# Performance work log

Measured on AMD Instinct MI355X. Metric: run time of the kernel, lower is better.

Reference implementation:

```python
import jax, jax.numpy as jnp
import numpy as np


def _run_lstm(x, W, U, b, mask=None):
    """Keras-style LSTM returning final hidden state.
    x: [N, T, D] float; W: [D, 4u]; U: [u, 4u]; b: [4u]; mask: [N, T] bool or None.
    Gate order i, f, g(c), o as in Keras. Masked steps carry state through.
    """
    N, T, D = x.shape
    units = U.shape[0]
    xt = jnp.transpose(x, (1, 0, 2))  # [T, N, D]
    if mask is not None:
        mt = jnp.transpose(mask, (1, 0))[:, :, None]  # [T, N, 1]
        xs = (xt, mt)
    else:
        xs = xt

    def step(carry, inp):
        h, c = carry
        if mask is not None:
            x_t, m = inp
        else:
            x_t = inp
        z = x_t @ W + h @ U + b  # [N, 4u]
        i, f, g, o = jnp.split(z, 4, axis=-1)
        i = jax.nn.sigmoid(i)
        f = jax.nn.sigmoid(f)
        g = jnp.tanh(g)
        o = jax.nn.sigmoid(o)
        c_new = f * c + i * g
        h_new = o * jnp.tanh(c_new)
        if mask is not None:
            h_new = jnp.where(m, h_new, h)
            c_new = jnp.where(m, c_new, c)
        return (h_new, c_new), None

    h0 = jnp.zeros((N, units), dtype=x.dtype)
    c0 = jnp.zeros((N, units), dtype=x.dtype)
    (hT, _), _ = jax.lax.scan(step, (h0, c0), xs)
    return hT


def setup_inputs() -> dict:
    key = jax.random.key(0)
    ks = jax.random.split(key, 10)
    B, T, S, D = 256, 256, 20, 1
    U1, U2 = 32, 24  # inner / outer LSTM units
    sc = 0.1
    x = jax.random.normal(ks[0], (B, T, S, D), dtype=jnp.float32)
    lengths = jax.random.randint(ks[1], (B,), 1, T + 1, dtype=jnp.int32)
    Wi = jax.random.normal(ks[2], (D, 4 * U1), dtype=jnp.float32) * sc
    Ui = jax.random.normal(ks[3], (U1, 4 * U1), dtype=jnp.float32) * sc
    bi = jnp.zeros((4 * U1,), dtype=jnp.float32)
    Wo = jax.random.normal(ks[4], (U1, 4 * U2), dtype=jnp.float32) * sc
    Uo = jax.random.normal(ks[5], (U2, 4 * U2), dtype=jnp.float32) * sc
    bo = jnp.zeros((4 * U2,), dtype=jnp.float32)
    Wd = jax.random.normal(ks[6], (U2, 1), dtype=jnp.float32) * sc
    bd = jnp.zeros((1,), dtype=jnp.float32)
    return {"x": x, "lengths": lengths, "Wi": Wi, "Ui": Ui, "bi": bi,
            "Wo": Wo, "Uo": Uo, "bo": bo, "Wd": Wd, "bd": bd}


def reference(x, lengths, Wi, Ui, bi, Wo, Uo, bo, Wd, bd):
    B, T, S, D = x.shape
    # TimeDistributed(LSTM(32)): run inner LSTM over each outer step (inference, dropout off)
    rows = x.reshape(B * T, S, D)
    h_inner = _run_lstm(rows, Wi, Ui, bi)          # [B*T, 32]
    feats = h_inner.reshape(B, T, -1)              # [B, T, 32]
    # Outer LSTM(24) with ragged-length mask (Keras mask semantics: carry state)
    mask = jnp.arange(T)[None, :] < lengths[:, None]  # [B, T]
    h_outer = _run_lstm(feats, Wo, Uo, bo, mask)   # [B, 24]
    # Dense sigmoid head
    return jax.nn.sigmoid(h_outer @ Wd + bd)       # [B, 1]
```

## Files before the change

kernel.cpp:

```cpp
#include <hip/hip_runtime.h>

#define B_  256
#define T_  256
#define S_  20
#define U1  32
#define G1  128
#define U2  24
#define G2  96
#define NT  16

typedef __attribute__((ext_vector_type(8))) short short8;
typedef __attribute__((ext_vector_type(4))) float f32x4;
typedef __attribute__((ext_vector_type(2))) float f32x2;

#define KSIG  (-1.44269504f)
#define KTANH ( 2.88539008f)

__device__ __forceinline__ float sigmoidf_(float x) {
    return __builtin_amdgcn_rcpf(1.0f + __builtin_amdgcn_exp2f(x * KSIG));
}
__device__ __forceinline__ float tanhf_fast(float x) {
    return 1.0f - 2.0f * __builtin_amdgcn_rcpf(1.0f + __builtin_amdgcn_exp2f(x * KTANH));
}
__device__ __forceinline__ float dpp_xor1(float x) {
    return __int_as_float(__builtin_amdgcn_update_dpp(
        0, __float_as_int(x), 0xB1, 0xF, 0xF, true));
}
__device__ __forceinline__ f32x2 dexp2(f32x2 z, float k) {
    f32x2 t = z * k;
    f32x2 e;
    e.x = __builtin_amdgcn_exp2f(t.x);
    e.y = __builtin_amdgcn_exp2f(t.y);
    return e + 1.0f;
}
__device__ __forceinline__ void brcp4(f32x2 d01, f32x2 d23, f32x2& s01, f32x2& s23) {
    const f32x2 m = d01 * d23;
    f32x2 R;
    R.x = __builtin_amdgcn_rcpf(m.x);
    R.y = __builtin_amdgcn_rcpf(m.y);
    s01 = R * d23;
    s23 = R * d01;
}

__device__ __forceinline__ unsigned short f2bf(float a) {
    unsigned int u = __float_as_uint(a);
    u += 0x7FFFu + ((u >> 16) & 1u);
    return (unsigned short)(u >> 16);
}
__device__ __forceinline__ unsigned int pack2bf(float a, float b) {
    unsigned int ua = __float_as_uint(a); ua += 0x7FFFu + ((ua >> 16) & 1u);
    unsigned int ub = __float_as_uint(b); ub += 0x7FFFu + ((ub >> 16) & 1u);
    return (ua >> 16) | (ub & 0xFFFF0000u);
}
union frag_u { short8 v; unsigned int u[4]; };
union h2x  { unsigned int u32; _Float16 h[2]; };

__global__ __attribute__((amdgpu_flat_work_group_size(512, 512)))
__attribute__((amdgpu_waves_per_eu(2, 2)))
void fused_kernel(
    const float* __restrict__ x,
    const int*   __restrict__ lengths,
    const float* __restrict__ Wi,
    const float* __restrict__ Ui,
    const float* __restrict__ bi,
    const float* __restrict__ Wo,
    const float* __restrict__ Uo,
    const float* __restrict__ bo,
    const float* __restrict__ Wd,
    const float* __restrict__ bd,
    float* __restrict__ out)
{
    __shared__ __align__(16) _Float16      Pl[T_][G2];
    __shared__ __align__(16) unsigned short hbb[8][16][40];
    __shared__ unsigned int flags[NT];
    const int b    = blockIdx.x;
    const int len  = lengths[b];
    const int tid  = threadIdx.x;
    const int w    = __builtin_amdgcn_readfirstlane(tid >> 6);
    const int lane = tid & 63;
    const int q    = lane >> 4;
    const int n    = lane & 15;

    if (tid < NT) flags[tid] = 0;
    __syncthreads();

    if (w <= 3) __builtin_amdgcn_s_setprio(2);

    frag_u Bui[8];
#pragma unroll
    for (int tt = 0; tt < 8; ++tt)
#pragma unroll
        for (int k2 = 0; k2 < 4; ++k2)
            Bui[tt].u[k2] = pack2bf(Ui[(8 * q + 2 * k2) * G1 + 16 * tt + n],
                                    Ui[(8 * q + 2 * k2 + 1) * G1 + 16 * tt + n]);
    frag_u Bwo[6];
#pragma unroll
    for (int tt = 0; tt < 6; ++tt)
#pragma unroll
        for (int k2 = 0; k2 < 4; ++k2)
            Bwo[tt].u[k2] = pack2bf(Wo[(8 * q + 2 * k2) * G2 + 16 * tt + n],
                                    Wo[(8 * q + 2 * k2 + 1) * G2 + 16 * tt + n]);
    float bi_l[8], Wi_l[8], bo_l[6];
#pragma unroll
    for (int tt = 0; tt < 8; ++tt) { bi_l[tt] = bi[16 * tt + n]; Wi_l[tt] = Wi[16 * tt + n]; }
#pragma unroll
    for (int tt = 0; tt < 6; ++tt) bo_l[tt] = bo[16 * tt + n];
    int pcol[6];
#pragma unroll
    for (int tt = 0; tt < 6; ++tt) {
        const int col = 16 * tt + n;
        const int g = col / 24;
        pcol[tt] = (col - 24 * g) * 4 + g;
    }

    int tl[3]; int ntl;
    if (w == 0)      { tl[0] = 0; tl[1] = 0; tl[2] = 0; ntl = 1; }
    else if (w == 1) { tl[0] = 1; tl[1] = 8; tl[2] = 9; ntl = 3; }
    else             { tl[0] = w; tl[1] = w + 8; tl[2] = 0; ntl = 2; }

#pragma unroll 1
    for (int i = 0; i < ntl; ++i) {
        const int tile = tl[i];
        const int wt0  = tile * 16;
        if (wt0 >= len) break;

        const float* xr = x + (size_t)(b * T_ + wt0 + 4 * q) * S_;
        f32x2 c01[2], c23[2];
#pragma unroll
        for (int uh = 0; uh < 2; ++uh) { c01[uh] = {0.0f, 0.0f}; c23[uh] = {0.0f, 0.0f}; }

        auto activate = [&](f32x4* acc) {
#pragma unroll
            for (int uh = 0; uh < 2; ++uh) {
                const f32x2 zi01 = { acc[0 + uh][0], acc[0 + uh][1] };
                const f32x2 zi23 = { acc[0 + uh][2], acc[0 + uh][3] };
                const f32x2 zf01 = { acc[2 + uh][0], acc[2 + uh][1] };
                const f32x2 zf23 = { acc[2 + uh][2], acc[2 + uh][3] };
                const f32x2 zg01 = { acc[4 + uh][0], acc[4 + uh][1] };
                const f32x2 zg23 = { acc[4 + uh][2], acc[4 + uh][3] };
                const f32x2 zo01 = { acc[6 + uh][0], acc[6 + uh][1] };
                const f32x2 zo23 = { acc[6 + uh][2], acc[6 + uh][3] };

                f32x2 si01, si23, sf01, sf23, rg01, rg23, so01, so23;
                brcp4(dexp2(zi01, KSIG),  dexp2(zi23, KSIG),  si01, si23);
                brcp4(dexp2(zf01, KSIG),  dexp2(zf23, KSIG),  sf01, sf23);
                brcp4(dexp2(zg01, KTANH), dexp2(zg23, KTANH), rg01, rg23);
                brcp4(dexp2(zo01, KSIG),  dexp2(zo23, KSIG),  so01, so23);
                const f32x2 g01 = 1.0f - 2.0f * rg01;
                const f32x2 g23 = 1.0f - 2.0f * rg23;
                c01[uh] = sf01 * c01[uh] + si01 * g01;
                c23[uh] = sf23 * c23[uh] + si23 * g23;
                f32x2 rc01, rc23;
                brcp4(dexp2(c01[uh], KTANH), dexp2(c23[uh], KTANH), rc01, rc23);
                const f32x2 t01 = 1.0f - 2.0f * rc01;
                const f32x2 t23 = 1.0f - 2.0f * rc23;
                const f32x2 h01 = so01 * t01;
                const f32x2 h23 = so23 * t23;
                hbb[w][4 * q + 0][n + 16 * uh] = f2bf(h01.x);
                hbb[w][4 * q + 1][n + 16 * uh] = f2bf(h01.y);
                hbb[w][4 * q + 2][n + 16 * uh] = f2bf(h23.x);
                hbb[w][4 * q + 3][n + 16 * uh] = f2bf(h23.y);
            }
        };

        float xc[4];
#pragma unroll
        for (int r = 0; r < 4; ++r) xc[r] = xr[r * S_];

        {
            f32x4 acc[8];
#pragma unroll
            for (int tt = 0; tt < 8; ++tt)
#pragma unroll
                for (int r = 0; r < 4; ++r)
                    acc[tt][r] = bi_l[tt] + xc[r] * Wi_l[tt];
            activate(acc);
        }
#pragma unroll
        for (int r = 0; r < 4; ++r) xc[r] = xr[r * S_ + 1];

#pragma unroll 1
        for (int s = 1; s < S_; ++s) {
            const int sn = (s + 1 < S_) ? s + 1 : S_ - 1;
            float xnx[4];
#pragma unroll
            for (int r = 0; r < 4; ++r) xnx[r] = xr[r * S_ + sn];

            f32x4 acc[8];
#pragma unroll
            for (int tt = 0; tt < 8; ++tt)
#pragma unroll
                for (int r = 0; r < 4; ++r)
                    acc[tt][r] = bi_l[tt] + xc[r] * Wi_l[tt];

            const short8 A = *(const short8*)&hbb[w][n][8 * q];
#pragma unroll
            for (int tt = 0; tt < 8; ++tt)
                acc[tt] = __builtin_amdgcn_mfma_f32_16x16x32_bf16(A, Bui[tt].v, acc[tt], 0, 0, 0);

            activate(acc);
#pragma unroll
            for (int r = 0; r < 4; ++r) xc[r] = xnx[r];
        }

        {
            const short8 A = *(const short8*)&hbb[w][n][8 * q];
            f32x4 accp[6];
#pragma unroll
            for (int tt = 0; tt < 6; ++tt) {
#pragma unroll
                for (int r = 0; r < 4; ++r) accp[tt][r] = bo_l[tt];
                accp[tt] = __builtin_amdgcn_mfma_f32_16x16x32_bf16(A, Bwo[tt].v, accp[tt], 0, 0, 0);
            }
#pragma unroll
            for (int r = 0; r < 4; ++r) {
                const int tr = wt0 + 4 * q + r;
#pragma unroll
                for (int tt = 0; tt < 6; ++tt)
                    Pl[tr][pcol[tt]] = (_Float16)accp[tt][r];
            }
        }
        __hip_atomic_store(&flags[tile], 1u, __ATOMIC_RELEASE, __HIP_MEMORY_SCOPE_WORKGROUP);
        if (i == 0) {
            if (w == 0) __builtin_amdgcn_s_setprio(1);
            else        __builtin_amdgcn_s_setprio(0);
        }
    }

    if (w != 0) return;

    const int p = lane & 1;
    const int u = (lane < 2 * U2) ? (lane >> 1) : (U2 - 1);
    const int cA = p ? (2 * U2 + u) : u;
    const int cB = p ? (3 * U2 + u) : (U2 + u);

    const f32x2 kAB = { p ? KTANH : KSIG, KSIG };
    const f32x2 mAB = { p ? -2.0f : 1.0f, 1.0f };
    const f32x2 aAB = { p ?  1.0f : 0.0f, 0.0f };

    auto gates2 = [&](f32x2 z) -> f32x2 {
        const f32x2 t = z * kAB;
        f32x2 e;
        e.x = __builtin_amdgcn_exp2f(t.x);
        e.y = __builtin_amdgcn_exp2f(t.y);
        const f32x2 d = e + 1.0f;
        f32x2 r;
        r.x = __builtin_amdgcn_rcpf(d.x);
        r.y = __builtin_amdgcn_rcpf(d.y);
        return r * mAB + aAB;
    };

    f32x2 w2_[U2];
#pragma unroll
    for (int k = 0; k < U2; ++k) {
        w2_[k].x = Uo[k * G2 + cA];
        w2_[k].y = Uo[k * G2 + cB];
    }

    const int rowoff = 8 * u + 4 * p;
    const char* Pb = reinterpret_cast<const char*>(&Pl[0][0]);
    const int ntiles = (len + 15) >> 4;

    unsigned bufA[16], bufB[16];

    float cu = 0.0f, hu = 0.0f;

#define STEP_ROW(RW) do {                                                     \
    h2x s_; s_.u32 = (RW);                                                    \
    f32x2 pr; pr.x = (float)s_.h[0]; pr.y = (float)s_.h[1];                   \
    float hk[U2];                                                             \
    _Pragma("unroll")                                                         \
    for (int kq = 0; kq < U2; ++kq)                                           \
        hk[kq] = __int_as_float(                                              \
            __builtin_amdgcn_readlane(__float_as_int(hu), 2 * kq + 1));       \
    f32x2 ab0 = pr;                                                           \
    f32x2 ab1 = {0.0f, 0.0f}, ab2 = {0.0f, 0.0f}, ab3 = {0.0f, 0.0f};         \
    _Pragma("unroll")                                                         \
    for (int kq = 0; kq < U2; kq += 4) {                                      \
        ab0 += w2_[kq]     * hk[kq];                                          \
        ab1 += w2_[kq + 1] * hk[kq + 1];                                      \
        ab2 += w2_[kq + 2] * hk[kq + 2];                                      \
        ab3 += w2_[kq + 3] * hk[kq + 3];                                      \
    }                                                                         \
    const f32x2 zz = (ab0 + ab1) + (ab2 + ab3);                               \
    const f32x2 o2 = gates2(zz);                                              \
    const float tg  = dpp_xor1(o2.x);                                         \
    cu = o2.y * cu + o2.x * tg;                                               \
    const float tc  = tanhf_fast(cu);                                         \
    const float tcs = dpp_xor1(tc);                                           \
    hu = o2.y * tcs;                                                          \
} while (0)

#define TILE_BODY(K, CUR, NXT, J0) do {                                       \
    _Pragma("unroll")                                                         \
    for (int j = (J0); j < 8; ++j) {                                          \
        if (16 * (K) + j >= len) goto p2done;                                 \
        STEP_ROW(CUR[j]);                                                     \
    }                                                                         \
    if ((K) + 1 < ntiles) {                                                   \
        while (__hip_atomic_load(&flags[(K) + 1], __ATOMIC_ACQUIRE,           \
                                 __HIP_MEMORY_SCOPE_WORKGROUP) == 0u)         \
            __builtin_amdgcn_s_sleep(1);                                      \
        _Pragma("unroll")                                                     \
        for (int j = 0; j < 16; ++j)                                          \
            NXT[j] = *reinterpret_cast<const unsigned*>(                      \
                Pb + (16 * ((K) + 1) + j) * (G2 * 2) + rowoff);               \
    }                                                                         \
    _Pragma("unroll")                                                         \
    for (int j = 8; j < 16; ++j) {                                            \
        if (16 * (K) + j >= len) goto p2done;                                 \
        STEP_ROW(CUR[j]);                                                     \
    }                                                                         \
} while (0)

#pragma unroll
    for (int j = 0; j < 16; ++j)
        bufA[j] = *reinterpret_cast<const unsigned*>(Pb + j * (G2 * 2) + rowoff);

    {
        h2x s_; s_.u32 = bufA[0];
        f32x2 z0; z0.x = (float)s_.h[0]; z0.y = (float)s_.h[1];
        const f32x2 o2 = gates2(z0);
        const float tg  = dpp_xor1(o2.x);
        cu = o2.x * tg;
        const float tc  = tanhf_fast(cu);
        const float tcs = dpp_xor1(tc);
        hu = o2.y * tcs;
    }

    TILE_BODY(0, bufA, bufB, 1);
#pragma unroll 1
    for (int k = 1; k < ntiles; ++k) {
        if (k & 1) TILE_BODY(k, bufB, bufA, 0);
        else       TILE_BODY(k, bufA, bufB, 0);
    }
p2done: ;

    float acc = bd[0];
#pragma unroll
    for (int k = 0; k < U2; ++k)
        acc += __int_as_float(__builtin_amdgcn_readlane(__float_as_int(hu), 2 * k + 1)) * Wd[k];
    if (lane == 0) out[b] = sigmoidf_(acc);

#undef TILE_BODY
#undef STEP_ROW
}

extern "C" void kernel_launch(void* const* d_in, const int* in_sizes, int n_in,
                              void* d_out, int out_size, void* d_ws, size_t ws_size,
                              hipStream_t stream) {
    const float* x       = (const float*)d_in[0];
    const int*   lengths = (const int*)  d_in[1];
    const float* Wi      = (const float*)d_in[2];
    const float* Ui      = (const float*)d_in[3];
    const float* bi      = (const float*)d_in[4];
    const float* Wo      = (const float*)d_in[5];
    const float* Uo      = (const float*)d_in[6];
    const float* bo      = (const float*)d_in[7];
    const float* Wd      = (const float*)d_in[8];
    const float* bd      = (const float*)d_in[9];
    float* out = (float*)d_out;

    fused_kernel<<<dim3(B_), dim3(512), 0, stream>>>(
        x, lengths, Wi, Ui, bi, Wo, Uo, bo, Wd, bd, out);
}
```

Before: 149.3 us.

## Fold exp2 scale constants into outer LSTM weights and shorten recurrent critical path

The outer LSTM step now pre-multiplies the recurrent weights and the projected inputs by the exp2 scale constants, so each gate's exponent is the accumulated sum directly. The cell state is kept pre-scaled by the tanh constant, and the output-gate swap is done in parallel with the cell-gate swap rather than after the tanh. This removes multiplies from the serial per-timestep dependency chain. The dot product uses eight accumulators instead of four, the inner-LSTM tile assignment across waves is reshuffled, wave 0's priority is raised, and the input projection uses packed float2 math. Precision shifts slightly because the scaled values are rounded differently.

Result: faster. 144.6 us (-3.1%).

```diff
diff --git a/kernel.cpp b/kernel.cpp
--- a/kernel.cpp
+++ b/kernel.cpp
@@ -114,9 +114,9 @@
     }
 
     int tl[3]; int ntl;
-    if (w == 0)      { tl[0] = 0; tl[1] = 0; tl[2] = 0; ntl = 1; }
-    else if (w == 1) { tl[0] = 1; tl[1] = 8; tl[2] = 9; ntl = 3; }
-    else             { tl[0] = w; tl[1] = w + 8; tl[2] = 0; ntl = 2; }
+    if (w == 0)      { tl[0] = 0; tl[1] = 0;  tl[2] = 0;  ntl = 1; }
+    else if (w == 7) { tl[0] = 7; tl[1] = 14; tl[2] = 15; ntl = 3; }
+    else             { tl[0] = w; tl[1] = w + 7; tl[2] = 0; ntl = 2; }
 
 #pragma unroll 1
     for (int i = 0; i < ntl; ++i) {
@@ -168,12 +168,15 @@
         for (int r = 0; r < 4; ++r) xc[r] = xr[r * S_];
 
         {
+            const f32x2 xc01 = { xc[0], xc[1] }, xc23 = { xc[2], xc[3] };
             f32x4 acc[8];
 #pragma unroll
-            for (int tt = 0; tt < 8; ++tt)
-#pragma unroll
-                for (int r = 0; r < 4; ++r)
-                    acc[tt][r] = bi_l[tt] + xc[r] * Wi_l[tt];
+            for (int tt = 0; tt < 8; ++tt) {
+                const f32x2 a01 = xc01 * Wi_l[tt] + bi_l[tt];
+                const f32x2 a23 = xc23 * Wi_l[tt] + bi_l[tt];
+                acc[tt][0] = a01.x; acc[tt][1] = a01.y;
+                acc[tt][2] = a23.x; acc[tt][3] = a23.y;
+            }
             activate(acc);
         }
 #pragma unroll
@@ -186,12 +189,15 @@
 #pragma unroll
             for (int r = 0; r < 4; ++r) xnx[r] = xr[r * S_ + sn];
 
+            const f32x2 xc01 = { xc[0], xc[1] }, xc23 = { xc[2], xc[3] };
             f32x4 acc[8];
 #pragma unroll
-            for (int tt = 0; tt < 8; ++tt)
-#pragma unroll
-                for (int r = 0; r < 4; ++r)
-                    acc[tt][r] = bi_l[tt] + xc[r] * Wi_l[tt];
+            for (int tt = 0; tt < 8; ++tt) {
+                const f32x2 a01 = xc01 * Wi_l[tt] + bi_l[tt];
+                const f32x2 a23 = xc23 * Wi_l[tt] + bi_l[tt];
+                acc[tt][0] = a01.x; acc[tt][1] = a01.y;
+                acc[tt][2] = a23.x; acc[tt][3] = a23.y;
+            }
 
             const short8 A = *(const short8*)&hbb[w][n][8 * q];
 #pragma unroll
@@ -222,7 +228,7 @@
         }
         __hip_atomic_store(&flags[tile], 1u, __ATOMIC_RELEASE, __HIP_MEMORY_SCOPE_WORKGROUP);
         if (i == 0) {
-            if (w == 0) __builtin_amdgcn_s_setprio(1);
+            if (w == 0) __builtin_amdgcn_s_setprio(3);
             else        __builtin_amdgcn_s_setprio(0);
         }
     }
@@ -234,28 +240,23 @@
     const int cA = p ? (2 * U2 + u) : u;
     const int cB = p ? (3 * U2 + u) : (U2 + u);
 
-    const f32x2 kAB = { p ? KTANH : KSIG, KSIG };
-    const f32x2 mAB = { p ? -2.0f : 1.0f, 1.0f };
-    const f32x2 aAB = { p ?  1.0f : 0.0f, 0.0f };
-
-    auto gates2 = [&](f32x2 z) -> f32x2 {
-        const f32x2 t = z * kAB;
-        f32x2 e;
-        e.x = __builtin_amdgcn_exp2f(t.x);
-        e.y = __builtin_amdgcn_exp2f(t.y);
-        const f32x2 d = e + 1.0f;
-        f32x2 r;
-        r.x = __builtin_amdgcn_rcpf(d.x);
-        r.y = __builtin_amdgcn_rcpf(d.y);
-        return r * mAB + aAB;
+    const float kx = p ? KTANH : KSIG;
+    const f32x2 kv  = { kx, KSIG };
+    const f32x2 mAB = { p ? (-2.0f * KTANH) : 1.0f, 1.0f };
+    const f32x2 aAB = { p ? KTANH : 0.0f, 0.0f };
+
+    f32x2 w2_[U2];
+#pragma unroll
+    for (int k = 0; k < U2; ++k) {
+        w2_[k].x = Uo[k * G2 + cA] * kx;
+        w2_[k].y = Uo[k * G2 + cB] * KSIG;
+    }
+
+    auto cvt2 = [&](unsigned rw) -> f32x2 {
+        h2x s_; s_.u32 = rw;
+        f32x2 r; r.x = (float)s_.h[0]; r.y = (float)s_.h[1];
+        return r * kv;
     };
-
-    f32x2 w2_[U2];
-#pragma unroll
-    for (int k = 0; k < U2; ++k) {
-        w2_[k].x = Uo[k * G2 + cA];
-        w2_[k].y = Uo[k * G2 + cB];
-    }
 
     const int rowoff = 8 * u + 4 * p;
     const char* Pb = reinterpret_cast<const char*>(&Pl[0][0]);
@@ -263,32 +264,46 @@
 
     unsigned bufA[16], bufB[16];
 
-    float cu = 0.0f, hu = 0.0f;
+    float cs = 0.0f, hu = 0.0f;
 
 #define STEP_ROW(RW) do {                                                     \
-    h2x s_; s_.u32 = (RW);                                                    \
-    f32x2 pr; pr.x = (float)s_.h[0]; pr.y = (float)s_.h[1];                   \
+    const f32x2 pr = cvt2(RW);                                                \
     float hk[U2];                                                             \
     _Pragma("unroll")                                                         \
     for (int kq = 0; kq < U2; ++kq)                                           \
         hk[kq] = __int_as_float(                                              \
-            __builtin_amdgcn_readlane(__float_as_int(hu), 2 * kq + 1));       \
+            __builtin_amdgcn_readlane(__float_as_int(hu), 2 * kq));           \
     f32x2 ab0 = pr;                                                           \
-    f32x2 ab1 = {0.0f, 0.0f}, ab2 = {0.0f, 0.0f}, ab3 = {0.0f, 0.0f};         \
+    f32x2 ab1 = {0.f,0.f}, ab2 = {0.f,0.f}, ab3 = {0.f,0.f};                  \
+    f32x2 ab4 = {0.f,0.f}, ab5 = {0.f,0.f}, ab6 = {0.f,0.f}, ab7 = {0.f,0.f}; \
     _Pragma("unroll")                                                         \
-    for (int kq = 0; kq < U2; kq += 4) {                                      \
-        ab0 += w2_[kq]     * hk[kq];                                          \
-        ab1 += w2_[kq + 1] * hk[kq + 1];                                      \
-        ab2 += w2_[kq + 2] * hk[kq + 2];                                      \
-        ab3 += w2_[kq + 3] * hk[kq + 3];                                      \
+    for (int mq = 0; mq < 3; ++mq) {                                          \
+        ab0 += w2_[8 * mq + 0] * hk[8 * mq + 0];                              \
+        ab1 += w2_[8 * mq + 1] * hk[8 * mq + 1];                              \
+        ab2 += w2_[8 * mq + 2] * hk[8 * mq + 2];                              \
+        ab3 += w2_[8 * mq + 3] * hk[8 * mq + 3];                              \
+        ab4 += w2_[8 * mq + 4] * hk[8 * mq + 4];                              \
+        ab5 += w2_[8 * mq + 5] * hk[8 * mq + 5];                              \
+        ab6 += w2_[8 * mq + 6] * hk[8 * mq + 6];                              \
+        ab7 += w2_[8 * mq + 7] * hk[8 * mq + 7];                              \
     }                                                                         \
-    const f32x2 zz = (ab0 + ab1) + (ab2 + ab3);                               \
-    const f32x2 o2 = gates2(zz);                                              \
-    const float tg  = dpp_xor1(o2.x);                                         \
-    cu = o2.y * cu + o2.x * tg;                                               \
-    const float tc  = tanhf_fast(cu);                                         \
-    const float tcs = dpp_xor1(tc);                                           \
-    hu = o2.y * tcs;                                                          \
+    const f32x2 zz = (((ab0 + ab1) + (ab2 + ab3)) +                           \
+                      ((ab4 + ab5) + (ab6 + ab7)));                           \
+    f32x2 e_;                                                                 \
+    e_.x = __builtin_amdgcn_exp2f(zz.x);                                      \
+    e_.y = __builtin_amdgcn_exp2f(zz.y);                                      \
+    const f32x2 d_ = e_ + 1.0f;                                               \
+    f32x2 r_;                                                                 \
+    r_.x = __builtin_amdgcn_rcpf(d_.x);                                       \
+    r_.y = __builtin_amdgcn_rcpf(d_.y);                                       \
+    const f32x2 o2 = r_ * mAB + aAB;                                          \
+    const float swx = dpp_xor1(o2.x);                 \
+    const float swy = dpp_xor1(o2.y);                  \
+    cs = o2.y * cs + o2.x * swx;                    \
+    const float e2 = __builtin_amdgcn_exp2f(cs);                              \
+    const float r2 = __builtin_amdgcn_rcpf(1.0f + e2);                        \
+    const float tc = 1.0f - 2.0f * r2;                   \
+    hu = swy * tc;                                      \
 } while (0)
 
 #define TILE_BODY(K, CUR, NXT, J0) do {                                       \
@@ -318,14 +333,22 @@
         bufA[j] = *reinterpret_cast<const unsigned*>(Pb + j * (G2 * 2) + rowoff);
 
     {
-        h2x s_; s_.u32 = bufA[0];
-        f32x2 z0; z0.x = (float)s_.h[0]; z0.y = (float)s_.h[1];
-        const f32x2 o2 = gates2(z0);
-        const float tg  = dpp_xor1(o2.x);
-        cu = o2.x * tg;
-        const float tc  = tanhf_fast(cu);
-        const float tcs = dpp_xor1(tc);
-        hu = o2.y * tcs;
+        const f32x2 z0 = cvt2(bufA[0]);
+        f32x2 e_;
+        e_.x = __builtin_amdgcn_exp2f(z0.x);
+        e_.y = __builtin_amdgcn_exp2f(z0.y);
+        const f32x2 d_ = e_ + 1.0f;
+        f32x2 r_;
+        r_.x = __builtin_amdgcn_rcpf(d_.x);
+        r_.y = __builtin_amdgcn_rcpf(d_.y);
+        const f32x2 o2 = r_ * mAB + aAB;
+        const float swx = dpp_xor1(o2.x);
+        const float swy = dpp_xor1(o2.y);
+        cs = o2.x * swx;
+        const float e2 = __builtin_amdgcn_exp2f(cs);
+        const float r2 = __builtin_amdgcn_rcpf(1.0f + e2);
+        const float tc = 1.0f - 2.0f * r2;
+        hu = swy * tc;
     }
 
     TILE_BODY(0, bufA, bufB, 1);
@@ -339,7 +362,7 @@
     float acc = bd[0];
 #pragma unroll
     for (int k = 0; k < U2; ++k)
-        acc += __int_as_float(__builtin_amdgcn_readlane(__float_as_int(hu), 2 * k + 1)) * Wd[k];
+        acc += __int_as_float(__builtin_amdgcn_readlane(__float_as_int(hu), 2 * k)) * Wd[k];
     if (lane == 0) out[b] = sigmoidf_(acc);
 
 #undef TILE_BODY
```
